# Performance work log

Measured on AMD Instinct MI355X. Metric: run time of the kernel, lower is better.

## Reference

```python
import jax, jax.numpy as jnp
import numpy as np

NUM_POSES = 200
N = 1048576

def _exp_vector(w):
    # Rodrigues formula: so(3) vector [N,3] -> rotation matrix [N,3,3]
    theta2 = jnp.sum(w * w, axis=-1)                     # [N]
    theta = jnp.sqrt(theta2 + 1e-12)                     # safe norm
    a = (jnp.sin(theta) / theta)[:, None, None]          # sin(t)/t
    b = ((1.0 - jnp.cos(theta)) / theta2.clip(1e-12))[:, None, None]
    wx, wy, wz = w[:, 0], w[:, 1], w[:, 2]
    zero = jnp.zeros_like(wx)
    K = jnp.stack([
        jnp.stack([zero, -wz, wy], axis=-1),
        jnp.stack([wz, zero, -wx], axis=-1),
        jnp.stack([-wy, wx, zero], axis=-1),
    ], axis=-2)                                          # [N,3,3] skew
    I = jnp.eye(3, dtype=w.dtype)
    return I + a * K + b * jnp.einsum('nij,njk->nik', K, K)

def setup_inputs() -> dict:
    key = jax.random.key(0)
    k1, k2, k3, k4 = jax.random.split(key, 4)
    n = jax.random.randint(k1, (N,), 0, NUM_POSES, dtype=jnp.int64)
    E = jax.random.normal(k2, (N, 4, 4), dtype=jnp.float32)
    R = jax.random.normal(k3, (NUM_POSES, 3), dtype=jnp.float32) * 0.1
    T = jax.random.normal(k4, (NUM_POSES, 3), dtype=jnp.float32) * 0.1
    return {"n": n, "E": E, "R": R, "T": T}

def reference(n, E, R, T):
    # mode == 'camera': pose = n
    Rg = R[n]                                            # [N,3] gather
    Tg = T[n]                                            # [N,3]
    rot = _exp_vector(Rg)                                # [N,3,3]
    top = jnp.concatenate([rot, Tg[:, :, None]], axis=2) # [N,3,4]
    bottom = jnp.broadcast_to(
        jnp.array([[0., 0., 0., 1.]], dtype=E.dtype)[None], (n.shape[0], 1, 4))
    M = jnp.concatenate([top, bottom], axis=1)           # [N,4,4]
    return jnp.einsum('nij,njk->nik', M, E)
```

## Files before the change

kernel.cpp:

```cpp
#include <hip/hip_runtime.h>

#define NUM_POSES 200

__device__ __forceinline__ float bf2f(unsigned int u16) {
    union { unsigned int u; float f; } v; v.u = u16 << 16; return v.f;
}
__device__ __forceinline__ unsigned int f2bf(float f) {
    union { float f; unsigned int u; } v; v.f = f;
    unsigned int r = v.u + 0x7FFFu + ((v.u >> 16) & 1u);
    return r >> 16;
}

__global__ void detect_kernel(const unsigned short* __restrict__ E16,
                              const unsigned int* __restrict__ n32,
                              int* __restrict__ flags) {
    __shared__ unsigned int sany;
    int t = threadIdx.x;
    if (t == 0) sany = 0u;
    __syncthreads();
    unsigned int local = 0u;
    for (int k = t; k < 4096; k += 256) {
        float a = fabsf(bf2f(E16[k]));
        if (!(a <= 1e6f)) local |= 1u;
    }
    if (t < 256 && n32[2 * t + 1] != 0u) local |= 2u;
    if (local) atomicOr(&sany, local);
    __syncthreads();
    if (t == 0) {
        flags[0] = (sany & 1u) ? 1 : 0;
        flags[1] = (sany & 2u) ? 1 : 0;
    }
}

__global__ void pose_kernel(const void* __restrict__ Rv,
                            const void* __restrict__ Tv,
                            const int* __restrict__ flags,
                            float* __restrict__ M) {
    int p = threadIdx.x;
    if (p >= NUM_POSES) return;
    float wx, wy, wz, tx, ty, tz;
    if (flags[0]) {
        const float* R = (const float*)Rv; const float* T = (const float*)Tv;
        wx = R[3*p+0]; wy = R[3*p+1]; wz = R[3*p+2];
        tx = T[3*p+0]; ty = T[3*p+1]; tz = T[3*p+2];
    } else {
        const unsigned short* R = (const unsigned short*)Rv;
        const unsigned short* T = (const unsigned short*)Tv;
        wx = bf2f(R[3*p+0]); wy = bf2f(R[3*p+1]); wz = bf2f(R[3*p+2]);
        tx = bf2f(T[3*p+0]); ty = bf2f(T[3*p+1]); tz = bf2f(T[3*p+2]);
    }
    float t2 = wx*wx + wy*wy + wz*wz;
    float th = sqrtf(t2 + 1e-12f);
    float a  = sinf(th) / th;
    float b  = (1.0f - cosf(th)) / fmaxf(t2, 1e-12f);

    float* m = M + p * 16;
    m[0]  = 1.0f - b * (wy*wy + wz*wz);
    m[1]  = -a * wz + b * wx * wy;
    m[2]  =  a * wy + b * wx * wz;
    m[3]  = tx;
    m[4]  =  a * wz + b * wx * wy;
    m[5]  = 1.0f - b * (wx*wx + wz*wz);
    m[6]  = -a * wx + b * wy * wz;
    m[7]  = ty;
    m[8]  = -a * wy + b * wx * wz;
    m[9]  =  a * wx + b * wy * wz;
    m[10] = 1.0f - b * (wx*wx + wy*wy);
    m[11] = tz;
    m[12] = 0.0f; m[13] = 0.0f; m[14] = 0.0f; m[15] = 1.0f;
}

__global__ __launch_bounds__(256) void apply_kernel(
        const void* __restrict__ nin,
        const void* __restrict__ Ein,
        const float4* __restrict__ M,
        void* __restrict__ outv,
        const int* __restrict__ flags,
        int N) {
    int i = blockIdx.x * blockDim.x + threadIdx.x;
    if (i >= N) return;
    const int e_is_f32 = flags[0];
    const int n_is_i32 = flags[1];

    long long p = n_is_i32 ? (long long)((const int*)nin)[i]
                           : ((const long long*)nin)[i];
    float4 m0 = M[p * 4 + 0];
    float4 m1 = M[p * 4 + 1];
    float4 m2 = M[p * 4 + 2];

    if (e_is_f32) {
        const float4* Ef = (const float4*)Ein + 4 * (size_t)i;
        float4 e0 = Ef[0], e1 = Ef[1], e2 = Ef[2], e3 = Ef[3];
        float4 r0, r1, r2;
        r0.x = m0.x*e0.x + m0.y*e1.x + m0.z*e2.x + m0.w*e3.x;
        r0.y = m0.x*e0.y + m0.y*e1.y + m0.z*e2.y + m0.w*e3.y;
        r0.z = m0.x*e0.z + m0.y*e1.z + m0.z*e2.z + m0.w*e3.z;
        r0.w = m0.x*e0.w + m0.y*e1.w + m0.z*e2.w + m0.w*e3.w;
        r1.x = m1.x*e0.x + m1.y*e1.x + m1.z*e2.x + m1.w*e3.x;
        r1.y = m1.x*e0.y + m1.y*e1.y + m1.z*e2.y + m1.w*e3.y;
        r1.z = m1.x*e0.z + m1.y*e1.z + m1.z*e2.z + m1.w*e3.z;
        r1.w = m1.x*e0.w + m1.y*e1.w + m1.z*e2.w + m1.w*e3.w;
        r2.x = m2.x*e0.x + m2.y*e1.x + m2.z*e2.x + m2.w*e3.x;
        r2.y = m2.x*e0.y + m2.y*e1.y + m2.z*e2.y + m2.w*e3.y;
        r2.z = m2.x*e0.z + m2.y*e1.z + m2.z*e2.z + m2.w*e3.z;
        r2.w = m2.x*e0.w + m2.y*e1.w + m2.z*e2.w + m2.w*e3.w;
        float4* Of = (float4*)outv + 4 * (size_t)i;
        Of[0] = r0; Of[1] = r1; Of[2] = r2; Of[3] = e3;
    } else {
        const uint4* Eb = (const uint4*)Ein + 2 * (size_t)i;
        uint4 e0 = Eb[0];
        uint4 e1 = Eb[1];
        float E00 = bf2f(e0.x & 0xFFFFu), E01 = bf2f(e0.x >> 16);
        float E02 = bf2f(e0.y & 0xFFFFu), E03 = bf2f(e0.y >> 16);
        float E10 = bf2f(e0.z & 0xFFFFu), E11 = bf2f(e0.z >> 16);
        float E12 = bf2f(e0.w & 0xFFFFu), E13 = bf2f(e0.w >> 16);
        float E20 = bf2f(e1.x & 0xFFFFu), E21 = bf2f(e1.x >> 16);
        float E22 = bf2f(e1.y & 0xFFFFu), E23 = bf2f(e1.y >> 16);
        float E30 = bf2f(e1.z & 0xFFFFu), E31 = bf2f(e1.z >> 16);
        float E32 = bf2f(e1.w & 0xFFFFu), E33 = bf2f(e1.w >> 16);

        float o00 = m0.x*E00 + m0.y*E10 + m0.z*E20 + m0.w*E30;
        float o01 = m0.x*E01 + m0.y*E11 + m0.z*E21 + m0.w*E31;
        float o02 = m0.x*E02 + m0.y*E12 + m0.z*E22 + m0.w*E32;
        float o03 = m0.x*E03 + m0.y*E13 + m0.z*E23 + m0.w*E33;
        float o10 = m1.x*E00 + m1.y*E10 + m1.z*E20 + m1.w*E30;
        float o11 = m1.x*E01 + m1.y*E11 + m1.z*E21 + m1.w*E31;
        float o12 = m1.x*E02 + m1.y*E12 + m1.z*E22 + m1.w*E32;
        float o13 = m1.x*E03 + m1.y*E13 + m1.z*E23 + m1.w*E33;
        float o20 = m2.x*E00 + m2.y*E10 + m2.z*E20 + m2.w*E30;
        float o21 = m2.x*E01 + m2.y*E11 + m2.z*E21 + m2.w*E31;
        float o22 = m2.x*E02 + m2.y*E12 + m2.z*E22 + m2.w*E32;
        float o23 = m2.x*E03 + m2.y*E13 + m2.z*E23 + m2.w*E33;

        uint4 r0, r1;
        r0.x = f2bf(o00) | (f2bf(o01) << 16);
        r0.y = f2bf(o02) | (f2bf(o03) << 16);
        r0.z = f2bf(o10) | (f2bf(o11) << 16);
        r0.w = f2bf(o12) | (f2bf(o13) << 16);
        r1.x = f2bf(o20) | (f2bf(o21) << 16);
        r1.y = f2bf(o22) | (f2bf(o23) << 16);
        r1.z = e1.z;
        r1.w = e1.w;
        uint4* Ob = (uint4*)outv + 2 * (size_t)i;
        Ob[0] = r0; Ob[1] = r1;
    }
}

extern "C" void kernel_launch(void* const* d_in, const int* in_sizes, int n_in,
                              void* d_out, int out_size, void* d_ws, size_t ws_size,
                              hipStream_t stream) {
    const void* n = d_in[0];
    const void* E = d_in[1];
    const void* R = d_in[2];
    const void* T = d_in[3];
    int*    flags = (int*)d_ws;
    float*      M = (float*)((char*)d_ws + 256);
    const int   N = in_sizes[0];

    detect_kernel<<<1, 256, 0, stream>>>((const unsigned short*)E,
                                         (const unsigned int*)n, flags);
    pose_kernel<<<1, 256, 0, stream>>>(R, T, flags, M);
    apply_kernel<<<(N + 255) / 256, 256, 0, stream>>>(
        n, E, (const float4*)M, d_out, flags, N);
}
```

Measured before the change: 141.0 us.

## Merge detect and pose kernels; map one thread per output row with shuffles

Fuses the dtype-detection and pose-matrix kernels into a single prep kernel, removing one launch. The apply kernel now uses four threads per 4x4 element, one per row. Each thread loads one E row with fully coalesced accesses and gathers the other rows by wavefront shuffles. This raises parallelism and improves coalescing of E loads and output stores, at the cost of 16 shuffles per thread, redundant index loads, and four times as many threads.

Result: faster. 134.4 us (-4.7%).

```diff
diff --git a/kernel.cpp b/kernel.cpp
--- a/kernel.cpp
+++ b/kernel.cpp
@@ -11,9 +11,21 @@
     return r >> 16;
 }
 
-__global__ void detect_kernel(const unsigned short* __restrict__ E16,
-                              const unsigned int* __restrict__ n32,
-                              int* __restrict__ flags) {
+__device__ __forceinline__ float4 shfl4(float4 v, int src) {
+    float4 r;
+    r.x = __shfl(v.x, src);
+    r.y = __shfl(v.y, src);
+    r.z = __shfl(v.z, src);
+    r.w = __shfl(v.w, src);
+    return r;
+}
+
+__global__ void prep_kernel(const unsigned short* __restrict__ E16,
+                            const unsigned int* __restrict__ n32,
+                            const void* __restrict__ Rv,
+                            const void* __restrict__ Tv,
+                            int* __restrict__ flags,
+                            float* __restrict__ M) {
     __shared__ unsigned int sany;
     int t = threadIdx.x;
     if (t == 0) sany = 0u;
@@ -23,23 +35,18 @@
         float a = fabsf(bf2f(E16[k]));
         if (!(a <= 1e6f)) local |= 1u;
     }
-    if (t < 256 && n32[2 * t + 1] != 0u) local |= 2u;
+    if (n32[2 * t + 1] != 0u) local |= 2u;
     if (local) atomicOr(&sany, local);
     __syncthreads();
+    unsigned int s = sany;
     if (t == 0) {
-        flags[0] = (sany & 1u) ? 1 : 0;
-        flags[1] = (sany & 2u) ? 1 : 0;
+        flags[0] = (s & 1u) ? 1 : 0;
+        flags[1] = (s & 2u) ? 1 : 0;
     }
-}
-
-__global__ void pose_kernel(const void* __restrict__ Rv,
-                            const void* __restrict__ Tv,
-                            const int* __restrict__ flags,
-                            float* __restrict__ M) {
-    int p = threadIdx.x;
-    if (p >= NUM_POSES) return;
+    if (t >= NUM_POSES) return;
+    int p = t;
     float wx, wy, wz, tx, ty, tz;
-    if (flags[0]) {
+    if (s & 1u) {
         const float* R = (const float*)Rv; const float* T = (const float*)Tv;
         wx = R[3*p+0]; wy = R[3*p+1]; wz = R[3*p+2];
         tx = T[3*p+0]; ty = T[3*p+1]; tz = T[3*p+2];
@@ -77,72 +84,48 @@
         void* __restrict__ outv,
         const int* __restrict__ flags,
         int N) {
-    int i = blockIdx.x * blockDim.x + threadIdx.x;
-    if (i >= N) return;
+    int t = blockIdx.x * blockDim.x + threadIdx.x;
+    int e = t >> 2;
+    int r = t & 3;
+    if (e >= N) return;
     const int e_is_f32 = flags[0];
     const int n_is_i32 = flags[1];
 
-    long long p = n_is_i32 ? (long long)((const int*)nin)[i]
-                           : ((const long long*)nin)[i];
-    float4 m0 = M[p * 4 + 0];
-    float4 m1 = M[p * 4 + 1];
-    float4 m2 = M[p * 4 + 2];
+    long long p = n_is_i32 ? (long long)((const int*)nin)[e]
+                           : ((const long long*)nin)[e];
+    float4 m = M[p * 4 + r];
+    int lb = (threadIdx.x & 63) & ~3;
 
     if (e_is_f32) {
-        const float4* Ef = (const float4*)Ein + 4 * (size_t)i;
-        float4 e0 = Ef[0], e1 = Ef[1], e2 = Ef[2], e3 = Ef[3];
-        float4 r0, r1, r2;
-        r0.x = m0.x*e0.x + m0.y*e1.x + m0.z*e2.x + m0.w*e3.x;
-        r0.y = m0.x*e0.y + m0.y*e1.y + m0.z*e2.y + m0.w*e3.y;
-        r0.z = m0.x*e0.z + m0.y*e1.z + m0.z*e2.z + m0.w*e3.z;
-        r0.w = m0.x*e0.w + m0.y*e1.w + m0.z*e2.w + m0.w*e3.w;
-        r1.x = m1.x*e0.x + m1.y*e1.x + m1.z*e2.x + m1.w*e3.x;
-        r1.y = m1.x*e0.y + m1.y*e1.y + m1.z*e2.y + m1.w*e3.y;
-        r1.z = m1.x*e0.z + m1.y*e1.z + m1.z*e2.z + m1.w*e3.z;
-        r1.w = m1.x*e0.w + m1.y*e1.w + m1.z*e2.w + m1.w*e3.w;
-        r2.x = m2.x*e0.x + m2.y*e1.x + m2.z*e2.x + m2.w*e3.x;
-        r2.y = m2.x*e0.y + m2.y*e1.y + m2.z*e2.y + m2.w*e3.y;
-        r2.z = m2.x*e0.z + m2.y*e1.z + m2.z*e2.z + m2.w*e3.z;
-        r2.w = m2.x*e0.w + m2.y*e1.w + m2.z*e2.w + m2.w*e3.w;
-        float4* Of = (float4*)outv + 4 * (size_t)i;
-        Of[0] = r0; Of[1] = r1; Of[2] = r2; Of[3] = e3;
+        float4 myrow = ((const float4*)Ein)[t];
+        float4 E0 = shfl4(myrow, lb + 0);
+        float4 E1 = shfl4(myrow, lb + 1);
+        float4 E2 = shfl4(myrow, lb + 2);
+        float4 E3 = shfl4(myrow, lb + 3);
+        float4 o;
+        o.x = m.x*E0.x + m.y*E1.x + m.z*E2.x + m.w*E3.x;
+        o.y = m.x*E0.y + m.y*E1.y + m.z*E2.y + m.w*E3.y;
+        o.z = m.x*E0.z + m.y*E1.z + m.z*E2.z + m.w*E3.z;
+        o.w = m.x*E0.w + m.y*E1.w + m.z*E2.w + m.w*E3.w;
+        ((float4*)outv)[t] = o;
     } else {
-        const uint4* Eb = (const uint4*)Ein + 2 * (size_t)i;
-        uint4 e0 = Eb[0];
-        uint4 e1 = Eb[1];
-        float E00 = bf2f(e0.x & 0xFFFFu), E01 = bf2f(e0.x >> 16);
-        float E02 = bf2f(e0.y & 0xFFFFu), E03 = bf2f(e0.y >> 16);
-        float E10 = bf2f(e0.z & 0xFFFFu), E11 = bf2f(e0.z >> 16);
-        float E12 = bf2f(e0.w & 0xFFFFu), E13 = bf2f(e0.w >> 16);
-        float E20 = bf2f(e1.x & 0xFFFFu), E21 = bf2f(e1.x >> 16);
-        float E22 = bf2f(e1.y & 0xFFFFu), E23 = bf2f(e1.y >> 16);
-        float E30 = bf2f(e1.z & 0xFFFFu), E31 = bf2f(e1.z >> 16);
-        float E32 = bf2f(e1.w & 0xFFFFu), E33 = bf2f(e1.w >> 16);
-
-        float o00 = m0.x*E00 + m0.y*E10 + m0.z*E20 + m0.w*E30;
-        float o01 = m0.x*E01 + m0.y*E11 + m0.z*E21 + m0.w*E31;
-        float o02 = m0.x*E02 + m0.y*E12 + m0.z*E22 + m0.w*E32;
-        float o03 = m0.x*E03 + m0.y*E13 + m0.z*E23 + m0.w*E33;
-        float o10 = m1.x*E00 + m1.y*E10 + m1.z*E20 + m1.w*E30;
-        float o11 = m1.x*E01 + m1.y*E11 + m1.z*E21 + m1.w*E31;
-        float o12 = m1.x*E02 + m1.y*E12 + m1.z*E22 + m1.w*E32;
-        float o13 = m1.x*E03 + m1.y*E13 + m1.z*E23 + m1.w*E33;
-        float o20 = m2.x*E00 + m2.y*E10 + m2.z*E20 + m2.w*E30;
-        float o21 = m2.x*E01 + m2.y*E11 + m2.z*E21 + m2.w*E31;
-        float o22 = m2.x*E02 + m2.y*E12 + m2.z*E22 + m2.w*E32;
-        float o23 = m2.x*E03 + m2.y*E13 + m2.z*E23 + m2.w*E33;
-
-        uint4 r0, r1;
-        r0.x = f2bf(o00) | (f2bf(o01) << 16);
-        r0.y = f2bf(o02) | (f2bf(o03) << 16);
-        r0.z = f2bf(o10) | (f2bf(o11) << 16);
-        r0.w = f2bf(o12) | (f2bf(o13) << 16);
-        r1.x = f2bf(o20) | (f2bf(o21) << 16);
-        r1.y = f2bf(o22) | (f2bf(o23) << 16);
-        r1.z = e1.z;
-        r1.w = e1.w;
-        uint4* Ob = (uint4*)outv + 2 * (size_t)i;
-        Ob[0] = r0; Ob[1] = r1;
+        uint2 raw = ((const uint2*)Ein)[t];
+        float4 myrow;
+        myrow.x = bf2f(raw.x & 0xFFFFu); myrow.y = bf2f(raw.x >> 16);
+        myrow.z = bf2f(raw.y & 0xFFFFu); myrow.w = bf2f(raw.y >> 16);
+        float4 E0 = shfl4(myrow, lb + 0);
+        float4 E1 = shfl4(myrow, lb + 1);
+        float4 E2 = shfl4(myrow, lb + 2);
+        float4 E3 = shfl4(myrow, lb + 3);
+        float4 o;
+        o.x = m.x*E0.x + m.y*E1.x + m.z*E2.x + m.w*E3.x;
+        o.y = m.x*E0.y + m.y*E1.y + m.z*E2.y + m.w*E3.y;
+        o.z = m.x*E0.z + m.y*E1.z + m.z*E2.z + m.w*E3.z;
+        o.w = m.x*E0.w + m.y*E1.w + m.z*E2.w + m.w*E3.w;
+        uint2 pk;
+        pk.x = f2bf(o.x) | (f2bf(o.y) << 16);
+        pk.y = f2bf(o.z) | (f2bf(o.w) << 16);
+        ((uint2*)outv)[t] = pk;
     }
 }
 
@@ -157,9 +140,9 @@
     float*      M = (float*)((char*)d_ws + 256);
     const int   N = in_sizes[0];
 
-    detect_kernel<<<1, 256, 0, stream>>>((const unsigned short*)E,
-                                         (const unsigned int*)n, flags);
-    pose_kernel<<<1, 256, 0, stream>>>(R, T, flags, M);
-    apply_kernel<<<(N + 255) / 256, 256, 0, stream>>>(
+    prep_kernel<<<1, 256, 0, stream>>>((const unsigned short*)E,
+                                       (const unsigned int*)n, R, T, flags, M);
+    const int rows = N * 4;
+    apply_kernel<<<(rows + 255) / 256, 256, 0, stream>>>(
         n, E, (const float4*)M, d_out, flags, N);
 }
```
